# Kernel tuning notes

Hardware: AMD Instinct MI355X
Metric: run time of the kernel (lower is better)

## Reference

```python
import jax, jax.numpy as jnp
import numpy as np

N = 50000        # nodes
E = 1_600_000    # edges
G = 64           # graphs in batch
IN = 10          # raw node feature width
XS, XE = 4, 10   # bus slice -> in_dim = 6
H = 256          # hidden_dim
OUT = 256        # out_dim
L = 3            # n_layers per expert
NE = 8           # n_experts
K = 2            # top_k


def _w(key, shape):
    fan_in = shape[-2] if len(shape) > 1 else shape[-1]
    return jax.random.normal(key, shape, jnp.float32) / np.sqrt(fan_in).astype(np.float32)


def setup_inputs() -> dict:
    key = jax.random.key(0)
    ks = jax.random.split(key, 18)
    x = jax.random.normal(ks[0], (N, IN), jnp.float32)
    edge_index = jax.random.randint(ks[1], (2, E), 0, N, dtype=jnp.int32)
    batch = jnp.sort(jax.random.randint(ks[2], (N,), 0, G, dtype=jnp.int32))
    return {
        "x": x,
        "edge_index": edge_index,
        "batch": batch,
        # SharedBusEncoder: Linear(in_dim, hidden) + ReLU
        "W_enc": _w(ks[3], (XE - XS, H)), "b_enc": jnp.zeros((H,), jnp.float32),
        # semantic BaseRouter: Linear(H,H)+ReLU+Linear(H,NE)
        "Ws1": _w(ks[4], (H, H)), "bs1": jnp.zeros((H,), jnp.float32),
        "Ws2": _w(ks[5], (H, NE)), "bs2": jnp.zeros((NE,), jnp.float32),
        # structural BaseRouter: Linear(2,H)+ReLU+Linear(H,NE)
        "Wt1": _w(ks[6], (2, H)), "bt1": jnp.zeros((H,), jnp.float32),
        "Wt2": _w(ks[7], (H, NE)), "bt2": jnp.zeros((NE,), jnp.float32),
        # GraphConvExpert stacks: x' = x@W_self + (sum_neighbors x)@W_neigh + b
        "W_self": _w(ks[8], (NE, L, H, OUT)),
        "W_neigh": _w(ks[9], (NE, L, H, OUT)),
        "b_exp": jnp.zeros((NE, L, OUT), jnp.float32),
    }


def reference(x, edge_index, batch, W_enc, b_enc, Ws1, bs1, Ws2, bs2,
              Wt1, bt1, Wt2, bt2, W_self, W_neigh, b_exp):
    src, dst = edge_index[0], edge_index[1]

    # SharedBusEncoder on bus feature slice
    h = jax.nn.relu(x[:, XS:XE] @ W_enc + b_enc)                       # [N, H]

    # graph_size_features: per-graph log node/edge counts, broadcast to nodes
    nodes_per_g = jax.ops.segment_sum(jnp.ones((N,), jnp.float32), batch, G)
    edges_per_g = jax.ops.segment_sum(jnp.ones((E,), jnp.float32), batch[src], G)
    size_feat = jnp.stack([jnp.log1p(nodes_per_g), jnp.log1p(edges_per_g)], -1)[batch]  # [N, 2]

    # dual routers, averaged
    sem = jax.nn.relu(h @ Ws1 + bs1) @ Ws2 + bs2                       # [N, NE]
    stru = jax.nn.relu(size_feat @ Wt1 + bt1) @ Wt2 + bt2              # [N, NE]
    logits = 0.5 * sem + 0.5 * stru

    # sparse_routing: softmax -> top-k mask -> renormalize (eval path, no noise)
    probs = jax.nn.softmax(logits, axis=-1)
    _, topi = jax.lax.top_k(probs, K)                                  # [N, K]
    mask = jnp.zeros_like(probs).at[jnp.arange(N)[:, None], topi].set(1.0)
    sp = probs * mask
    sparse = sp / jnp.sum(sp, axis=-1, keepdims=True)                  # [N, NE]

    # dense GraphConv experts over all nodes
    def run_expert(Ws, Wn, b):
        z = h
        for l in range(L):
            agg = jax.ops.segment_sum(z[src], dst, N)                  # neighbor sum
            z = z @ Ws[l] + agg @ Wn[l] + b[l]
            if l < L - 1:
                z = jax.nn.relu(z)
        return z                                                        # [N, OUT]

    y = jax.vmap(run_expert)(W_self, W_neigh, b_exp)                   # [NE, N, OUT]
    return jnp.einsum('end,ne->nd', y, sparse)                         # [N, OUT]
```

## Files before the change

### kernel.cpp

```cpp
#include <hip/hip_runtime.h>


#define NN 50000
#define EE 1600000
#define GG 64
#define HH 256
#define NEXP 8
#define LAY 3
#define KD 512
#define MT 128
#define BK 64
#define GB 391
#define AGB 6250
#define MPAD 50048L

typedef __attribute__((ext_vector_type(8))) short bf16x8;
typedef __attribute__((ext_vector_type(8))) unsigned short u16x8;
typedef __attribute__((ext_vector_type(4))) float f32x4;

__device__ __forceinline__ float bf2f(unsigned short u) {
    union { unsigned int i; float f; } v; v.i = ((unsigned int)u) << 16; return v.f;
}
__device__ __forceinline__ unsigned short f2bf(float f) {
    union { unsigned int i; float f; } v; v.f = f;
    unsigned int r = (v.i + 0x7FFFu + ((v.i >> 16) & 1u)) >> 16;
    return (unsigned short)r;
}
__device__ __forceinline__ void gll16(unsigned short* l, const unsigned short* g) {
    __builtin_amdgcn_global_load_lds((__attribute__((address_space(1))) void*)g,
                                     (__attribute__((address_space(3))) void*)l, 16, 0, 0);
}

__global__ void encoder_kernel(const float* __restrict__ x, const float* __restrict__ W,
                               const float* __restrict__ b, unsigned short* __restrict__ out) {
    int n = blockIdx.x, j = threadIdx.x;
    float acc = b[j];
#pragma unroll
    for (int i = 0; i < 6; i++) acc += x[n * 10 + 4 + i] * W[i * HH + j];
    acc = fmaxf(acc, 0.f);
    out[(long)n * KD + j] = f2bf(acc);
}

__global__ void pack_experts(const float* __restrict__ Wself, const float* __restrict__ Wneigh,
                             unsigned short* __restrict__ Bt) {
    int idx = blockIdx.x * 256 + threadIdx.x;
    int n = idx & 255; int r = idx >> 8;
    int k = r & 511; r >>= 9;
    int l = r % LAY; int e = r / LAY;
    float v = (k < 256) ? Wself[(((e * LAY + l) * HH) + k) * HH + n]
                        : Wneigh[(((e * LAY + l) * HH) + (k - 256)) * HH + n];
    Bt[(((long)(e * LAY + l) * HH + n) * KD) + k] = f2bf(v);
}

__global__ void pack_ws1(const float* __restrict__ W, unsigned short* __restrict__ Bt) {
    int idx = blockIdx.x * 256 + threadIdx.x;
    int n = idx & 255; int k = idx >> 8;
    Bt[(long)n * HH + k] = f2bf(W[k * HH + n]);
}

__global__ void deg2_kernel(const int* __restrict__ src, const int* __restrict__ dst,
                            const int* __restrict__ batch, int* __restrict__ deg,
                            unsigned short* __restrict__ perm, int* __restrict__ ecnt) {
    __shared__ int he[GG];
    if (threadIdx.x < GG) he[threadIdx.x] = 0;
    __syncthreads();
    int e = blockIdx.x * 256 + threadIdx.x;
    if (e < EE) {
        perm[e] = (unsigned short)atomicAdd(&deg[dst[e]], 1);
        atomicAdd(&he[batch[src[e]]], 1);
    }
    __syncthreads();
    if (threadIdx.x < GG && he[threadIdx.x]) atomicAdd(&ecnt[threadIdx.x], he[threadIdx.x]);
}

__global__ void stru_kernel(const int* __restrict__ batch, const int* __restrict__ ecnt,
                            const float* __restrict__ Wt1, const float* __restrict__ bt1,
                            const float* __restrict__ Wt2, const float* __restrict__ bt2,
                            float* __restrict__ strug) {
    __shared__ float t[HH];
    __shared__ int nc;
    int g = blockIdx.x, j = threadIdx.x;
    if (j == 0) {
        int lo = 0, hi = NN;
        while (lo < hi) { int mid = (lo + hi) >> 1; if (batch[mid] < g) lo = mid + 1; else hi = mid; }
        int s = lo; lo = 0; hi = NN;
        while (lo < hi) { int mid = (lo + hi) >> 1; if (batch[mid] < g + 1) lo = mid + 1; else hi = mid; }
        nc = lo - s;
    }
    __syncthreads();
    float nf = log1pf((float)nc);
    float ef = log1pf((float)ecnt[g]);
    float v = nf * Wt1[j] + ef * Wt1[HH + j] + bt1[j];
    t[j] = fmaxf(v, 0.f);
    __syncthreads();
    if (j < 8) {
        float sum = bt2[j];
        for (int k = 0; k < HH; k++) sum += t[k] * Wt2[k * 8 + j];
        strug[g * 8 + j] = sum;
    }
}

__global__ void scan_kernel(const int* __restrict__ deg, int* __restrict__ rowstart) {
    __shared__ int wsum[16];
    __shared__ int carry_s;
    int tid = threadIdx.x;
    int wid = tid >> 6, lane = tid & 63;
    if (tid == 0) carry_s = 0;
    __syncthreads();
    for (int base = 0; base < NN; base += 1024) {
        int i = base + tid;
        int v = (i < NN) ? deg[i] : 0;
        int sc = v;
#pragma unroll
        for (int off = 1; off < 64; off <<= 1) {
            int t = __shfl_up(sc, off, 64);
            if (lane >= off) sc += t;
        }
        if (lane == 63) wsum[wid] = sc;
        __syncthreads();
        int carry = carry_s;
        int prev = 0;
        for (int w = 0; w < wid; w++) prev += wsum[w];
        int excl = carry + prev + sc - v;
        if (i < NN) rowstart[i] = excl;
        __syncthreads();
        if (tid == 1023) carry_s = carry + prev + sc;
    }
    __syncthreads();
    if (tid == 0) rowstart[NN] = carry_s;
}

__global__ void scatter2_kernel(const int* __restrict__ src, const int* __restrict__ dst,
                                const unsigned short* __restrict__ perm,
                                const int* __restrict__ rowstart,
                                unsigned short* __restrict__ cols) {
    int e = blockIdx.x * 256 + threadIdx.x;
    if (e < EE) cols[rowstart[dst[e]] + (int)perm[e]] = (unsigned short)src[e];
}

__global__ void agg_kernel(unsigned short* __restrict__ base, long estride,
                           const int* __restrict__ rowstart, const unsigned short* __restrict__ cols,
                           const int* __restrict__ listp, const int* __restrict__ cntp) {
    const unsigned short* Z = base + (long)blockIdx.y * estride;
    unsigned short* Aout = base + (long)blockIdx.y * estride;
    int half = threadIdx.x >> 5;
    int lane = threadIdx.x & 31;
    int idx = blockIdx.x * 8 + half;
    int limit = cntp ? cntp[blockIdx.y] : NN;
    if (idx >= limit) return;
    int nid = listp ? (listp[(long)blockIdx.y * NN + idx] & 0xFFFF) : idx;
    int s = rowstart[nid], e = rowstart[nid + 1];
    float acc[8] = {0.f, 0.f, 0.f, 0.f, 0.f, 0.f, 0.f, 0.f};
    int i = s;
    for (; i + 8 <= e; i += 8) {
        int c[8];
#pragma unroll
        for (int u = 0; u < 8; u++) c[u] = (int)cols[i + u];
        u16x8 v[8];
#pragma unroll
        for (int u = 0; u < 8; u++) v[u] = *(const u16x8*)&Z[(long)c[u] * KD + lane * 8];
#pragma unroll
        for (int u = 0; u < 8; u++)
#pragma unroll
            for (int j = 0; j < 8; j++) acc[j] += bf2f(v[u][j]);
    }
    for (; i < e; i++) {
        int c = (int)cols[i];
        u16x8 v = *(const u16x8*)&Z[(long)c * KD + lane * 8];
#pragma unroll
        for (int j = 0; j < 8; j++) acc[j] += bf2f(v[j]);
    }
    u16x8 o;
#pragma unroll
    for (int j = 0; j < 8; j++) o[j] = f2bf(acc[j]);
    *(u16x8*)&Aout[(long)nid * KD + 256 + lane * 8] = o;
}

__global__ void route_kernel(const unsigned short* __restrict__ T, const float* __restrict__ Ws2,
                             const float* __restrict__ bs2, const float* __restrict__ strug,
                             const int* __restrict__ batch, float* __restrict__ sparse,
                             int* __restrict__ topi) {
    int nid = blockIdx.x * 4 + (threadIdx.x >> 6);
    if (nid >= NN) return;
    int lane = threadIdx.x & 63;
    float s[8];
#pragma unroll
    for (int j = 0; j < 8; j++) s[j] = 0.f;
    ushort4 t4 = *(const ushort4*)&T[(long)nid * HH + lane * 4];
    float tv[4] = { bf2f(t4.x), bf2f(t4.y), bf2f(t4.z), bf2f(t4.w) };
#pragma unroll
    for (int kk = 0; kk < 4; kk++) {
        int k = lane * 4 + kk;
#pragma unroll
        for (int j = 0; j < 8; j++) s[j] += tv[kk] * Ws2[k * 8 + j];
    }
#pragma unroll
    for (int off = 32; off >= 1; off >>= 1) {
#pragma unroll
        for (int j = 0; j < 8; j++) s[j] += __shfl_xor(s[j], off, 64);
    }
    int g = batch[nid];
    float p[8], mx = -1e30f;
#pragma unroll
    for (int j = 0; j < 8; j++) {
        p[j] = 0.5f * (s[j] + bs2[j] + strug[g * 8 + j]);
        mx = fmaxf(mx, p[j]);
    }
    float ex[8];
#pragma unroll
    for (int j = 0; j < 8; j++) ex[j] = expf(p[j] - mx);
    int i1 = 0;
#pragma unroll
    for (int j = 1; j < 8; j++) if (ex[j] > ex[i1]) i1 = j;
    int i2 = (i1 == 0) ? 1 : 0;
#pragma unroll
    for (int j = 0; j < 8; j++) if (j != i1 && ex[j] > ex[i2]) i2 = j;
    float r = 1.f / (ex[i1] + ex[i2]);
    if (lane == 0) topi[nid] = i1 | (i2 << 8);
    if (lane < 8)
        sparse[(long)nid * 8 + lane] = (lane == i1) ? ex[i1] * r : (lane == i2) ? ex[i2] * r : 0.f;
}

__global__ void build_lists(const float* __restrict__ sparse, const int* __restrict__ topi,
                            int* __restrict__ cnt, int* __restrict__ lists) {
    __shared__ int lc[NEXP], lb[NEXP];
    int tid = threadIdx.x;
    if (tid < NEXP) lc[tid] = 0;
    __syncthreads();
    int n = blockIdx.x * 256 + tid;
    int le_[2], pk_[2], ps_[2];
    int cc = 0;
    if (n < NN) {
        int t1 = topi[n] & 0xFF;
#pragma unroll
        for (int e = 0; e < NEXP; e++) {
            if (sparse[(long)n * 8 + e] > 0.f && cc < 2) {
                le_[cc] = e;
                pk_[cc] = n | ((e == t1) ? 0 : (1 << 16));
                ps_[cc] = atomicAdd(&lc[e], 1);
                cc++;
            }
        }
    }
    __syncthreads();
    if (tid < NEXP) lb[tid] = atomicAdd(&cnt[tid], lc[tid]);
    __syncthreads();
    for (int c = 0; c < cc; c++)
        lists[(long)le_[c] * NN + lb[le_[c]] + ps_[c]] = pk_[c];
}

template <int MODE>
__global__ __launch_bounds__(256, 2) void gemm_kernel(
    const unsigned short* __restrict__ A, long ae, int lda, int K,
    const unsigned short* __restrict__ Bt, long bte,
    const float* __restrict__ bias, int be_s,
    void* __restrict__ outp, long oe, int ldz,
    const float* __restrict__ sparse, int e0,
    const int* __restrict__ listp, const int* __restrict__ cntp) {
    __shared__ __align__(16) unsigned short Alds[MT * 64];
    __shared__ __align__(16) unsigned short Blds[HH * 64];
    __shared__ int nodeids[MT];
    const int el = blockIdx.y;
    const unsigned short* Ae = A + (long)el * ae;
    const unsigned short* Bte = Bt + (long)el * bte;
    const float* be = bias + (long)el * be_s;
    const int tid = threadIdx.x;
    const int wave = tid >> 6, lane = tid & 63;
    const int m = lane & 15, q = lane >> 4;
    const long row0 = (long)blockIdx.x * MT;

    if constexpr (MODE == 1) {
        int limit = cntp[el];
        if (row0 >= limit) return;
        if (tid < MT) {
            long rr = row0 + tid;
            nodeids[tid] = (rr < limit) ? listp[(long)el * NN + rr] : -1;
        }
        __syncthreads();
    }

    const unsigned short* asrc[4];
#pragma unroll
    for (int i = 0; i < 4; i++) {
        int slot = tid + 256 * i;
        int r = slot >> 3, cg = (slot & 7) ^ (r & 7);
        long arow;
        if constexpr (MODE == 0) {
            arow = row0 + r;
        } else {
            int v = nodeids[r];
            arow = (v >= 0) ? (v & 0xFFFF) : 0;
        }
        asrc[i] = Ae + arow * (long)lda + cg * 8;
    }
    const unsigned short* bsrc[8];
#pragma unroll
    for (int i = 0; i < 8; i++) {
        int slot = tid + 256 * i;
        int r = slot >> 3, cg = (slot & 7) ^ (r & 7);
        bsrc[i] = Bte + (long)r * K + cg * 8;
    }

    f32x4 acc[2][16];
#pragma unroll
    for (int i = 0; i < 2; i++)
#pragma unroll
        for (int j = 0; j < 16; j++) acc[i][j] = (f32x4){0.f, 0.f, 0.f, 0.f};

    const int swz = (m & 7) << 3;
    for (int k0 = 0; k0 < K; k0 += BK) {
#pragma unroll
        for (int i = 0; i < 4; i++) gll16(&Alds[(tid + 256 * i) * 8], asrc[i] + k0);
#pragma unroll
        for (int i = 0; i < 8; i++) gll16(&Blds[(tid + 256 * i) * 8], bsrc[i] + k0);
        __syncthreads();
#pragma unroll
        for (int kk = 0; kk < BK; kk += 32) {
            const int ch8 = (((kk >> 3) + q) << 3) ^ swz;
            const int ao = (wave * 32 + m) * 64 + ch8;
            bf16x8 a0 = *(const bf16x8*)&Alds[ao];
            bf16x8 a1 = *(const bf16x8*)&Alds[ao + 16 * 64];
#pragma unroll
            for (int ct = 0; ct < 16; ct++) {
                bf16x8 b = *(const bf16x8*)&Blds[(ct * 16 + m) * 64 + ch8];
                acc[0][ct] = __builtin_amdgcn_mfma_f32_16x16x32_bf16(a0, b, acc[0][ct], 0, 0, 0);
                acc[1][ct] = __builtin_amdgcn_mfma_f32_16x16x32_bf16(a1, b, acc[1][ct], 0, 0, 0);
            }
        }
        __syncthreads();
    }
#pragma unroll
    for (int mt = 0; mt < 2; mt++) {
        int rtile = wave * 32 + mt * 16 + q * 4;
        if constexpr (MODE == 0) {
            unsigned short* oute = (unsigned short*)outp + (long)el * oe;
            long rbase = row0 + rtile;
#pragma unroll
            for (int ct = 0; ct < 16; ct++) {
                int col = ct * 16 + m;
                float bv = be[col];
#pragma unroll
                for (int r = 0; r < 4; r++) {
                    long grow = rbase + r;
                    if (grow < NN) {
                        float v = fmaxf(acc[mt][ct][r] + bv, 0.f);
                        oute[grow * ldz + col] = f2bf(v);
                    }
                }
            }
        } else {
            unsigned short* outR = (unsigned short*)outp;
            int v4[4]; float w4[4];
#pragma unroll
            for (int r = 0; r < 4; r++) {
                v4[r] = nodeids[rtile + r];
                w4[r] = (v4[r] >= 0) ? sparse[(long)(v4[r] & 0xFFFF) * 8 + e0 + el] : 0.f;
            }
#pragma unroll
            for (int ct = 0; ct < 16; ct++) {
                int col = ct * 16 + m;
                float bv = be[col];
#pragma unroll
                for (int r = 0; r < 4; r++) {
                    if (v4[r] >= 0) {
                        long nid = v4[r] & 0xFFFF;
                        long rank = (v4[r] >> 16) & 1;
                        outR[(rank * MPAD + nid) * HH + col] = f2bf(w4[r] * (acc[mt][ct][r] + bv));
                    }
                }
            }
        }
    }
}

__global__ void combine_kernel(const unsigned short* __restrict__ outR, float* __restrict__ out) {
    long base = ((long)blockIdx.x * 256 + threadIdx.x) * 8;
    u16x8 r0 = *(const u16x8*)&outR[base];
    u16x8 r1 = *(const u16x8*)&outR[MPAD * HH + base];
    f32x4 lo, hi;
#pragma unroll
    for (int j = 0; j < 4; j++) lo[j] = bf2f(r0[j]) + bf2f(r1[j]);
#pragma unroll
    for (int j = 0; j < 4; j++) hi[j] = bf2f(r0[j + 4]) + bf2f(r1[j + 4]);
    *(f32x4*)&out[base] = lo;
    *(f32x4*)&out[base + 4] = hi;
}

extern "C" void kernel_launch(void* const* d_in, const int* in_sizes, int n_in,
                              void* d_out, int out_size, void* d_ws, size_t ws_size,
                              hipStream_t stream) {
    const float* x     = (const float*)d_in[0];
    const int*   ei    = (const int*)d_in[1];
    const int*   src   = ei;
    const int*   dst   = ei + EE;
    const int*   batch = (const int*)d_in[2];
    const float* W_enc = (const float*)d_in[3];
    const float* b_enc = (const float*)d_in[4];
    const float* Ws1   = (const float*)d_in[5];
    const float* bs1   = (const float*)d_in[6];
    const float* Ws2   = (const float*)d_in[7];
    const float* bs2   = (const float*)d_in[8];
    const float* Wt1   = (const float*)d_in[9];
    const float* bt1   = (const float*)d_in[10];
    const float* Wt2   = (const float*)d_in[11];
    const float* bt2   = (const float*)d_in[12];
    const float* W_self  = (const float*)d_in[13];
    const float* W_neigh = (const float*)d_in[14];
    const float* b_exp   = (const float*)d_in[15];
    float* out = (float*)d_out;

    char* ws = (char*)d_ws;
    size_t off = 0;
    auto alloc = [&](size_t b) { size_t p = off; off = (off + b + 255) & ~(size_t)255; return ws + p; };

    unsigned short* Ash  = (unsigned short*)alloc((size_t)MPAD * KD * 2);
    unsigned short* outR = (unsigned short*)alloc((size_t)2 * MPAD * HH * 2);
    unsigned short* Tbuf = outR;
    unsigned short* BtE = (unsigned short*)alloc((size_t)NEXP * LAY * HH * KD * 2);
    unsigned short* Bt1 = (unsigned short*)alloc((size_t)HH * HH * 2);
    float* sparse  = (float*)alloc((size_t)NN * 8 * 4);
    int* topi      = (int*)alloc((size_t)NN * 4);
    float* strug   = (float*)alloc((size_t)GG * 8 * 4);
    int* ecnt      = (int*)alloc((size_t)GG * 4);
    int* deg       = (int*)alloc((size_t)NN * 4);
    int* rowstart  = (int*)alloc((size_t)(NN + 1) * 4);
    unsigned short* perm = (unsigned short*)alloc((size_t)EE * 2);
    unsigned short* cols = (unsigned short*)alloc((size_t)EE * 2);
    int* lists     = (int*)alloc((size_t)NEXP * NN * 4);
    int* cnt8      = (int*)alloc((size_t)NEXP * 4);

    const long BUFS = MPAD * KD;
    long avail = ((long)ws_size - (long)off) / (BUFS * 2);
    int EG = (avail < 1) ? 1 : (avail > NEXP ? NEXP : (int)avail);
    unsigned short* bufs = (unsigned short*)(ws + off);

    hipMemsetAsync(ecnt, 0, GG * 4, stream);
    hipMemsetAsync(deg, 0, (size_t)NN * 4, stream);
    hipMemsetAsync(cnt8, 0, NEXP * 4, stream);

    pack_experts<<<NEXP * LAY * KD * HH / 256, 256, 0, stream>>>(W_self, W_neigh, BtE);
    pack_ws1<<<HH * HH / 256, 256, 0, stream>>>(Ws1, Bt1);
    encoder_kernel<<<NN, HH, 0, stream>>>(x, W_enc, b_enc, Ash);

    deg2_kernel<<<(EE + 255) / 256, 256, 0, stream>>>(src, dst, batch, deg, perm, ecnt);
    scan_kernel<<<1, 1024, 0, stream>>>(deg, rowstart);
    scatter2_kernel<<<(EE + 255) / 256, 256, 0, stream>>>(src, dst, perm, rowstart, cols);
    stru_kernel<<<GG, HH, 0, stream>>>(batch, ecnt, Wt1, bt1, Wt2, bt2, strug);

    gemm_kernel<0><<<dim3(GB, 1), 256, 0, stream>>>(Ash, 0, KD, HH, Bt1, 0, bs1, 0,
                                                    Tbuf, 0, HH, nullptr, 0, nullptr, nullptr);
    route_kernel<<<(NN + 3) / 4, 256, 0, stream>>>(Tbuf, Ws2, bs2, strug, batch, sparse, topi);
    build_lists<<<(NN + 255) / 256, 256, 0, stream>>>(sparse, topi, cnt8, lists);

    agg_kernel<<<dim3(AGB, 1), 256, 0, stream>>>(Ash, 0, rowstart, cols, nullptr, nullptr);

    const long BTL = (long)LAY * HH * KD;
    for (int e0 = 0; e0 < NEXP; e0 += EG) {
        int eg = (NEXP - e0 < EG) ? (NEXP - e0) : EG;
        dim3 gg(GB, eg), ga(AGB, eg);
        gemm_kernel<0><<<gg, 256, 0, stream>>>(Ash, 0, KD, KD,
                                               BtE + (size_t)(e0 * LAY + 0) * HH * KD, BTL,
                                               b_exp + (size_t)e0 * LAY * HH, LAY * HH,
                                               bufs, BUFS, KD, nullptr, 0, nullptr, nullptr);
        agg_kernel<<<ga, 256, 0, stream>>>(bufs, BUFS, rowstart, cols, nullptr, nullptr);
        gemm_kernel<0><<<gg, 256, 0, stream>>>(bufs, BUFS, KD, KD,
                                               BtE + (size_t)(e0 * LAY + 1) * HH * KD, BTL,
                                               b_exp + (size_t)e0 * LAY * HH + HH, LAY * HH,
                                               bufs, BUFS, KD, nullptr, 0, nullptr, nullptr);
        agg_kernel<<<ga, 256, 0, stream>>>(bufs, BUFS, rowstart, cols,
                                           lists + (size_t)e0 * NN, cnt8 + e0);
        gemm_kernel<1><<<gg, 256, 0, stream>>>(bufs, BUFS, KD, KD,
                                               BtE + (size_t)(e0 * LAY + 2) * HH * KD, BTL,
                                               b_exp + (size_t)e0 * LAY * HH + 2 * HH, LAY * HH,
                                               outR, 0, 0, sparse, e0,
                                               lists + (size_t)e0 * NN, cnt8 + e0);
    }
    combine_kernel<<<NN * HH / 8 / 256, 256, 0, stream>>>(outR, out);
}
```

Before: 2.168 ms.

## Fuse GEMM and aggregation blocks across experts into single launches with double buffering

Merges the GEMM and neighbour-aggregation kernels into one fused kernel whose blocks run either a GEMM tile or an aggregation row group, depending on block index. Experts are now processed one at a time with two ping-pong buffers. Independent work from the previous expert (its layer-2 aggregation and final routed GEMM) runs in the same launch as the current expert's GEMMs, as does the router GEMM with the first aggregation. The aim is to overlap the memory-bound gather with the compute-bound MFMA GEMM and cut kernel launches. In exchange, experts are no longer batched across grid.y, the GEMM mode becomes a runtime branch instead of a template, and the fused kernel's register and LDS budget is shared by both paths.

```diff
diff --git a/kernel.cpp b/kernel.cpp
--- a/kernel.cpp
+++ b/kernel.cpp
@@ -138,17 +138,17 @@
     if (e < EE) cols[rowstart[dst[e]] + (int)perm[e]] = (unsigned short)src[e];
 }
 
-__global__ void agg_kernel(unsigned short* __restrict__ base, long estride,
-                           const int* __restrict__ rowstart, const unsigned short* __restrict__ cols,
-                           const int* __restrict__ listp, const int* __restrict__ cntp) {
-    const unsigned short* Z = base + (long)blockIdx.y * estride;
-    unsigned short* Aout = base + (long)blockIdx.y * estride;
+__device__ __forceinline__ void agg_body(int bx, unsigned short* __restrict__ base,
+                                         const int* __restrict__ rowstart,
+                                         const unsigned short* __restrict__ cols,
+                                         const int* __restrict__ listp,
+                                         const int* __restrict__ cntp) {
     int half = threadIdx.x >> 5;
     int lane = threadIdx.x & 31;
-    int idx = blockIdx.x * 8 + half;
-    int limit = cntp ? cntp[blockIdx.y] : NN;
+    int idx = bx * 8 + half;
+    int limit = cntp ? *cntp : NN;
     if (idx >= limit) return;
-    int nid = listp ? (listp[(long)blockIdx.y * NN + idx] & 0xFFFF) : idx;
+    int nid = listp ? (listp[idx] & 0xFFFF) : idx;
     int s = rowstart[nid], e = rowstart[nid + 1];
     float acc[8] = {0.f, 0.f, 0.f, 0.f, 0.f, 0.f, 0.f, 0.f};
     int i = s;
@@ -158,7 +158,7 @@
         for (int u = 0; u < 8; u++) c[u] = (int)cols[i + u];
         u16x8 v[8];
 #pragma unroll
-        for (int u = 0; u < 8; u++) v[u] = *(const u16x8*)&Z[(long)c[u] * KD + lane * 8];
+        for (int u = 0; u < 8; u++) v[u] = *(const u16x8*)&base[(long)c[u] * KD + lane * 8];
 #pragma unroll
         for (int u = 0; u < 8; u++)
 #pragma unroll
@@ -166,14 +166,20 @@
     }
     for (; i < e; i++) {
         int c = (int)cols[i];
-        u16x8 v = *(const u16x8*)&Z[(long)c * KD + lane * 8];
+        u16x8 v = *(const u16x8*)&base[(long)c * KD + lane * 8];
 #pragma unroll
         for (int j = 0; j < 8; j++) acc[j] += bf2f(v[j]);
     }
     u16x8 o;
 #pragma unroll
     for (int j = 0; j < 8; j++) o[j] = f2bf(acc[j]);
-    *(u16x8*)&Aout[(long)nid * KD + 256 + lane * 8] = o;
+    *(u16x8*)&base[(long)nid * KD + 256 + lane * 8] = o;
+}
+
+__global__ void agg_kernel(unsigned short* __restrict__ base, const int* __restrict__ rowstart,
+                           const unsigned short* __restrict__ cols,
+                           const int* __restrict__ listp, const int* __restrict__ cntp) {
+    agg_body(blockIdx.x, base, rowstart, cols, listp, cntp);
 }
 
 __global__ void route_kernel(const unsigned short* __restrict__ T, const float* __restrict__ Ws2,
@@ -249,32 +255,27 @@
         lists[(long)le_[c] * NN + lb[le_[c]] + ps_[c]] = pk_[c];
 }
 
-template <int MODE>
-__global__ __launch_bounds__(256, 2) void gemm_kernel(
-    const unsigned short* __restrict__ A, long ae, int lda, int K,
-    const unsigned short* __restrict__ Bt, long bte,
-    const float* __restrict__ bias, int be_s,
-    void* __restrict__ outp, long oe, int ldz,
-    const float* __restrict__ sparse, int e0,
+__device__ __forceinline__ void gemm_body(
+    int bx, int mode,
+    const unsigned short* __restrict__ A, int lda, int K,
+    const unsigned short* __restrict__ Bt, const float* __restrict__ bias,
+    void* __restrict__ outp, int ldz,
+    const float* __restrict__ sparse, int expert,
     const int* __restrict__ listp, const int* __restrict__ cntp) {
     __shared__ __align__(16) unsigned short Alds[MT * 64];
     __shared__ __align__(16) unsigned short Blds[HH * 64];
     __shared__ int nodeids[MT];
-    const int el = blockIdx.y;
-    const unsigned short* Ae = A + (long)el * ae;
-    const unsigned short* Bte = Bt + (long)el * bte;
-    const float* be = bias + (long)el * be_s;
     const int tid = threadIdx.x;
     const int wave = tid >> 6, lane = tid & 63;
     const int m = lane & 15, q = lane >> 4;
-    const long row0 = (long)blockIdx.x * MT;
-
-    if constexpr (MODE == 1) {
-        int limit = cntp[el];
+    const long row0 = (long)bx * MT;
+
+    if (mode == 1) {
+        int limit = *cntp;
         if (row0 >= limit) return;
         if (tid < MT) {
             long rr = row0 + tid;
-            nodeids[tid] = (rr < limit) ? listp[(long)el * NN + rr] : -1;
+            nodeids[tid] = (rr < limit) ? listp[rr] : -1;
         }
         __syncthreads();
     }
@@ -285,20 +286,20 @@
         int slot = tid + 256 * i;
         int r = slot >> 3, cg = (slot & 7) ^ (r & 7);
         long arow;
-        if constexpr (MODE == 0) {
+        if (mode == 0) {
             arow = row0 + r;
         } else {
             int v = nodeids[r];
             arow = (v >= 0) ? (v & 0xFFFF) : 0;
         }
-        asrc[i] = Ae + arow * (long)lda + cg * 8;
+        asrc[i] = A + arow * (long)lda + cg * 8;
     }
     const unsigned short* bsrc[8];
 #pragma unroll
     for (int i = 0; i < 8; i++) {
         int slot = tid + 256 * i;
         int r = slot >> 3, cg = (slot & 7) ^ (r & 7);
-        bsrc[i] = Bte + (long)r * K + cg * 8;
+        bsrc[i] = Bt + (long)r * K + cg * 8;
     }
 
     f32x4 acc[2][16];
@@ -332,13 +333,13 @@
 #pragma unroll
     for (int mt = 0; mt < 2; mt++) {
         int rtile = wave * 32 + mt * 16 + q * 4;
-        if constexpr (MODE == 0) {
-            unsigned short* oute = (unsigned short*)outp + (long)el * oe;
+        if (mode == 0) {
+            unsigned short* oute = (unsigned short*)outp;
             long rbase = row0 + rtile;
 #pragma unroll
             for (int ct = 0; ct < 16; ct++) {
                 int col = ct * 16 + m;
-                float bv = be[col];
+                float bv = bias[col];
 #pragma unroll
                 for (int r = 0; r < 4; r++) {
                     long grow = rbase + r;
@@ -354,12 +355,12 @@
 #pragma unroll
             for (int r = 0; r < 4; r++) {
                 v4[r] = nodeids[rtile + r];
-                w4[r] = (v4[r] >= 0) ? sparse[(long)(v4[r] & 0xFFFF) * 8 + e0 + el] : 0.f;
+                w4[r] = (v4[r] >= 0) ? sparse[(long)(v4[r] & 0xFFFF) * 8 + expert] : 0.f;
             }
 #pragma unroll
             for (int ct = 0; ct < 16; ct++) {
                 int col = ct * 16 + m;
-                float bv = be[col];
+                float bv = bias[col];
 #pragma unroll
                 for (int r = 0; r < 4; r++) {
                     if (v4[r] >= 0) {
@@ -371,6 +372,22 @@
             }
         }
     }
+}
+
+__global__ __launch_bounds__(256, 2) void fused_kernel(
+    int gsplit, int gmode,
+    const unsigned short* __restrict__ A, int lda, int K,
+    const unsigned short* __restrict__ Bt, const float* __restrict__ bias,
+    void* __restrict__ outp, int ldz,
+    const float* __restrict__ sparse, int expert,
+    const int* __restrict__ glist, const int* __restrict__ gcnt,
+    unsigned short* __restrict__ abase,
+    const int* __restrict__ rowstart, const unsigned short* __restrict__ cols,
+    const int* __restrict__ alist, const int* __restrict__ acnt) {
+    if ((int)blockIdx.x < gsplit)
+        gemm_body(blockIdx.x, gmode, A, lda, K, Bt, bias, outp, ldz, sparse, expert, glist, gcnt);
+    else
+        agg_body(blockIdx.x - gsplit, abase, rowstart, cols, alist, acnt);
 }
 
 __global__ void combine_kernel(const unsigned short* __restrict__ outR, float* __restrict__ out) {
@@ -430,9 +447,7 @@
     int* cnt8      = (int*)alloc((size_t)NEXP * 4);
 
     const long BUFS = MPAD * KD;
-    long avail = ((long)ws_size - (long)off) / (BUFS * 2);
-    int EG = (avail < 1) ? 1 : (avail > NEXP ? NEXP : (int)avail);
-    unsigned short* bufs = (unsigned short*)(ws + off);
+    unsigned short* bufs = (unsigned short*)alloc((size_t)2 * BUFS * 2);
 
     hipMemsetAsync(ecnt, 0, GG * 4, stream);
     hipMemsetAsync(deg, 0, (size_t)NN * 4, stream);
@@ -447,33 +462,52 @@
     scatter2_kernel<<<(EE + 255) / 256, 256, 0, stream>>>(src, dst, perm, rowstart, cols);
     stru_kernel<<<GG, HH, 0, stream>>>(batch, ecnt, Wt1, bt1, Wt2, bt2, strug);
 
-    gemm_kernel<0><<<dim3(GB, 1), 256, 0, stream>>>(Ash, 0, KD, HH, Bt1, 0, bs1, 0,
-                                                    Tbuf, 0, HH, nullptr, 0, nullptr, nullptr);
+    fused_kernel<<<GB + AGB, 256, 0, stream>>>(
+        GB, 0, Ash, KD, HH, Bt1, bs1, Tbuf, HH, nullptr, 0, nullptr, nullptr,
+        Ash, rowstart, cols, nullptr, nullptr);
     route_kernel<<<(NN + 3) / 4, 256, 0, stream>>>(Tbuf, Ws2, bs2, strug, batch, sparse, topi);
     build_lists<<<(NN + 255) / 256, 256, 0, stream>>>(sparse, topi, cnt8, lists);
 
-    agg_kernel<<<dim3(AGB, 1), 256, 0, stream>>>(Ash, 0, rowstart, cols, nullptr, nullptr);
-
-    const long BTL = (long)LAY * HH * KD;
-    for (int e0 = 0; e0 < NEXP; e0 += EG) {
-        int eg = (NEXP - e0 < EG) ? (NEXP - e0) : EG;
-        dim3 gg(GB, eg), ga(AGB, eg);
-        gemm_kernel<0><<<gg, 256, 0, stream>>>(Ash, 0, KD, KD,
-                                               BtE + (size_t)(e0 * LAY + 0) * HH * KD, BTL,
-                                               b_exp + (size_t)e0 * LAY * HH, LAY * HH,
-                                               bufs, BUFS, KD, nullptr, 0, nullptr, nullptr);
-        agg_kernel<<<ga, 256, 0, stream>>>(bufs, BUFS, rowstart, cols, nullptr, nullptr);
-        gemm_kernel<0><<<gg, 256, 0, stream>>>(bufs, BUFS, KD, KD,
-                                               BtE + (size_t)(e0 * LAY + 1) * HH * KD, BTL,
-                                               b_exp + (size_t)e0 * LAY * HH + HH, LAY * HH,
-                                               bufs, BUFS, KD, nullptr, 0, nullptr, nullptr);
-        agg_kernel<<<ga, 256, 0, stream>>>(bufs, BUFS, rowstart, cols,
-                                           lists + (size_t)e0 * NN, cnt8 + e0);
-        gemm_kernel<1><<<gg, 256, 0, stream>>>(bufs, BUFS, KD, KD,
-                                               BtE + (size_t)(e0 * LAY + 2) * HH * KD, BTL,
-                                               b_exp + (size_t)e0 * LAY * HH + 2 * HH, LAY * HH,
-                                               outR, 0, 0, sparse, e0,
-                                               lists + (size_t)e0 * NN, cnt8 + e0);
+    for (int e = 0; e < NEXP; e++) {
+        unsigned short* buf  = bufs + (size_t)(e & 1) * BUFS;
+        unsigned short* pbuf = bufs + (size_t)((e + 1) & 1) * BUFS;
+        const unsigned short* B0 = BtE + (size_t)(e * LAY + 0) * HH * KD;
+        const unsigned short* B1 = BtE + (size_t)(e * LAY + 1) * HH * KD;
+        const float* bb = b_exp + (size_t)e * LAY * HH;
+        const unsigned short* B2p = BtE + (size_t)((e - 1) * LAY + 2) * HH * KD;
+        const float* bbp = b_exp + (size_t)(e - 1) * LAY * HH + 2 * HH;
+        const int* lp = lists + (size_t)(e - 1) * NN;
+        const int* cp = cnt8 + (e - 1);
+
+        if (e == 0) {
+            fused_kernel<<<GB, 256, 0, stream>>>(
+                GB, 0, Ash, KD, KD, B0, bb, buf, KD, nullptr, 0, nullptr, nullptr,
+                nullptr, rowstart, cols, nullptr, nullptr);
+        } else {
+            fused_kernel<<<GB + AGB, 256, 0, stream>>>(
+                GB, 0, Ash, KD, KD, B0, bb, buf, KD, nullptr, 0, nullptr, nullptr,
+                pbuf, rowstart, cols, lp, cp);
+        }
+        if (e == 0) {
+            agg_kernel<<<AGB, 256, 0, stream>>>(buf, rowstart, cols, nullptr, nullptr);
+        } else {
+            fused_kernel<<<GB + AGB, 256, 0, stream>>>(
+                GB, 1, pbuf, KD, KD, B2p, bbp, outR, 0, sparse, e - 1, lp, cp,
+                buf, rowstart, cols, nullptr, nullptr);
+        }
+        fused_kernel<<<GB, 256, 0, stream>>>(
+            GB, 0, buf, KD, KD, B1, bb + HH, buf, KD, nullptr, 0, nullptr, nullptr,
+            nullptr, rowstart, cols, nullptr, nullptr);
+    }
+    {
+        unsigned short* buf7 = bufs + (size_t)(7 & 1) * BUFS;
+        const int* lp = lists + (size_t)7 * NN;
+        const int* cp = cnt8 + 7;
+        agg_kernel<<<AGB, 256, 0, stream>>>(buf7, rowstart, cols, lp, cp);
+        fused_kernel<<<GB, 256, 0, stream>>>(
+            GB, 1, buf7, KD, KD, BtE + (size_t)(7 * LAY + 2) * HH * KD,
+            b_exp + (size_t)7 * LAY * HH + 2 * HH, outR, 0, sparse, 7, lp, cp,
+            nullptr, rowstart, cols, nullptr, nullptr);
     }
     combine_kernel<<<NN * HH / 8 / 256, 256, 0, stream>>>(outR, out);
 }
```

Result: slower. 2.379 ms (+9.7%).

## Slice aggregation by column chunks and split edge histogram into ballot kernel

Applied to the files above, without the earlier changes.

The neighbor aggregation kernel now gives each block 64 nodes and one of 8 column slices of 32 features, with 4 threads per node, in place of 8 nodes across all 256 columns. Blocks that share a slice touch the same 64-byte region of each gathered row, which is meant to improve cache locality for the random neighbor gathers. The per-edge degree/permutation pass is split from the graph edge-count histogram. The histogram now runs as a separate grid-stride kernel that counts with wavefront ballots, which avoids per-edge shared atomics but adds an extra pass over the edges. Each gathered row is now fetched as 8 separate 64-byte pieces, so there are more, smaller memory requests per edge.

```diff
diff --git a/kernel.cpp b/kernel.cpp
--- a/kernel.cpp
+++ b/kernel.cpp
@@ -11,7 +11,7 @@
 #define MT 128
 #define BK 64
 #define GB 391
-#define AGB 6250
+#define SLG 6256
 #define MPAD 50048L
 
 typedef __attribute__((ext_vector_type(8))) short bf16x8;
@@ -58,19 +58,33 @@
     Bt[(long)n * HH + k] = f2bf(W[k * HH + n]);
 }
 
-__global__ void deg2_kernel(const int* __restrict__ src, const int* __restrict__ dst,
-                            const int* __restrict__ batch, int* __restrict__ deg,
-                            unsigned short* __restrict__ perm, int* __restrict__ ecnt) {
-    __shared__ int he[GG];
-    if (threadIdx.x < GG) he[threadIdx.x] = 0;
-    __syncthreads();
+__global__ void degp_kernel(const int* __restrict__ dst, int* __restrict__ deg,
+                            unsigned short* __restrict__ perm) {
     int e = blockIdx.x * 256 + threadIdx.x;
-    if (e < EE) {
-        perm[e] = (unsigned short)atomicAdd(&deg[dst[e]], 1);
-        atomicAdd(&he[batch[src[e]]], 1);
-    }
-    __syncthreads();
-    if (threadIdx.x < GG && he[threadIdx.x]) atomicAdd(&ecnt[threadIdx.x], he[threadIdx.x]);
+    if (e < EE) perm[e] = (unsigned short)atomicAdd(&deg[dst[e]], 1);
+}
+
+#define HBLK 128
+#define HITER ((EE + HBLK * 256 - 1) / (HBLK * 256))
+__global__ void hist2_kernel(const int* __restrict__ src, const int* __restrict__ batch,
+                             int* __restrict__ ecnt) {
+    __shared__ int h[GG];
+    if (threadIdx.x < GG) h[threadIdx.x] = 0;
+    __syncthreads();
+    int lane = threadIdx.x & 63;
+    int gid = blockIdx.x * 256 + threadIdx.x;
+    int cnt = 0;
+    for (int it = 0; it < HITER; it++) {
+        long e = (long)it * (HBLK * 256) + gid;
+        int g = (e < EE) ? batch[src[e]] : -1;
+        for (int gg = 0; gg < GG; gg++) {
+            unsigned long long m = __ballot(g == gg);
+            if (lane == gg) cnt += (int)__popcll(m);
+        }
+    }
+    atomicAdd(&h[lane], cnt);
+    __syncthreads();
+    if (threadIdx.x < GG && h[threadIdx.x]) atomicAdd(&ecnt[threadIdx.x], h[threadIdx.x]);
 }
 
 __global__ void stru_kernel(const int* __restrict__ batch, const int* __restrict__ ecnt,
@@ -141,15 +155,17 @@
 __global__ void agg_kernel(unsigned short* __restrict__ base, long estride,
                            const int* __restrict__ rowstart, const unsigned short* __restrict__ cols,
                            const int* __restrict__ listp, const int* __restrict__ cntp) {
-    const unsigned short* Z = base + (long)blockIdx.y * estride;
-    unsigned short* Aout = base + (long)blockIdx.y * estride;
-    int half = threadIdx.x >> 5;
-    int lane = threadIdx.x & 31;
-    int idx = blockIdx.x * 8 + half;
+    unsigned short* Z = base + (long)blockIdx.y * estride;
+    const int slice = blockIdx.x & 7;
+    const int chunk = blockIdx.x >> 3;
+    const int grp = threadIdx.x >> 2, l4 = threadIdx.x & 3;
     int limit = cntp ? cntp[blockIdx.y] : NN;
+    if (chunk * 64 >= limit) return;
+    int idx = chunk * 64 + grp;
     if (idx >= limit) return;
     int nid = listp ? (listp[(long)blockIdx.y * NN + idx] & 0xFFFF) : idx;
     int s = rowstart[nid], e = rowstart[nid + 1];
+    const int co = slice * 32 + l4 * 8;
     float acc[8] = {0.f, 0.f, 0.f, 0.f, 0.f, 0.f, 0.f, 0.f};
     int i = s;
     for (; i + 8 <= e; i += 8) {
@@ -158,7 +174,7 @@
         for (int u = 0; u < 8; u++) c[u] = (int)cols[i + u];
         u16x8 v[8];
 #pragma unroll
-        for (int u = 0; u < 8; u++) v[u] = *(const u16x8*)&Z[(long)c[u] * KD + lane * 8];
+        for (int u = 0; u < 8; u++) v[u] = *(const u16x8*)&Z[(long)c[u] * KD + co];
 #pragma unroll
         for (int u = 0; u < 8; u++)
 #pragma unroll
@@ -166,14 +182,14 @@
     }
     for (; i < e; i++) {
         int c = (int)cols[i];
-        u16x8 v = *(const u16x8*)&Z[(long)c * KD + lane * 8];
+        u16x8 v = *(const u16x8*)&Z[(long)c * KD + co];
 #pragma unroll
         for (int j = 0; j < 8; j++) acc[j] += bf2f(v[j]);
     }
     u16x8 o;
 #pragma unroll
     for (int j = 0; j < 8; j++) o[j] = f2bf(acc[j]);
-    *(u16x8*)&Aout[(long)nid * KD + 256 + lane * 8] = o;
+    *(u16x8*)&Z[(long)nid * KD + 256 + co] = o;
 }
 
 __global__ void route_kernel(const unsigned short* __restrict__ T, const float* __restrict__ Ws2,
@@ -442,7 +458,8 @@
     pack_ws1<<<HH * HH / 256, 256, 0, stream>>>(Ws1, Bt1);
     encoder_kernel<<<NN, HH, 0, stream>>>(x, W_enc, b_enc, Ash);
 
-    deg2_kernel<<<(EE + 255) / 256, 256, 0, stream>>>(src, dst, batch, deg, perm, ecnt);
+    degp_kernel<<<(EE + 255) / 256, 256, 0, stream>>>(dst, deg, perm);
+    hist2_kernel<<<HBLK, 256, 0, stream>>>(src, batch, ecnt);
     scan_kernel<<<1, 1024, 0, stream>>>(deg, rowstart);
     scatter2_kernel<<<(EE + 255) / 256, 256, 0, stream>>>(src, dst, perm, rowstart, cols);
     stru_kernel<<<GG, HH, 0, stream>>>(batch, ecnt, Wt1, bt1, Wt2, bt2, strug);
@@ -452,12 +469,12 @@
     route_kernel<<<(NN + 3) / 4, 256, 0, stream>>>(Tbuf, Ws2, bs2, strug, batch, sparse, topi);
     build_lists<<<(NN + 255) / 256, 256, 0, stream>>>(sparse, topi, cnt8, lists);
 
-    agg_kernel<<<dim3(AGB, 1), 256, 0, stream>>>(Ash, 0, rowstart, cols, nullptr, nullptr);
+    agg_kernel<<<dim3(SLG, 1), 256, 0, stream>>>(Ash, 0, rowstart, cols, nullptr, nullptr);
 
     const long BTL = (long)LAY * HH * KD;
     for (int e0 = 0; e0 < NEXP; e0 += EG) {
         int eg = (NEXP - e0 < EG) ? (NEXP - e0) : EG;
-        dim3 gg(GB, eg), ga(AGB, eg);
+        dim3 gg(GB, eg), ga(SLG, eg);
         gemm_kernel<0><<<gg, 256, 0, stream>>>(Ash, 0, KD, KD,
                                                BtE + (size_t)(e0 * LAY + 0) * HH * KD, BTL,
                                                b_exp + (size_t)e0 * LAY * HH, LAY * HH,
```

Result: slower. 2.597 ms (+19.8%).
